# Kernel tuning notes

Measured on AMD Instinct MI355X. Metric: run time of the kernel, lower is better.

The kernel has to match this reference:

```python
import jax, jax.numpy as jnp
import numpy as np

N = 100000
E = 1600000
F_IN = 128
H = 256
C = 40
BN_EPS = 1e-5


def setup_inputs() -> dict:
    key = jax.random.key(0)
    ks = jax.random.split(key, 16)
    x = jax.random.normal(ks[0], (N, F_IN), dtype=jnp.float32)
    edge_index = jax.random.randint(ks[1], (2, E), 0, N, dtype=jnp.int64)
    # pre layer
    pre_w = jax.random.normal(ks[2], (H, F_IN), dtype=jnp.float32) * (1.0 / np.sqrt(F_IN))
    pre_b = jnp.zeros((H,), jnp.float32)
    # batchnorm params stacked [5, 4, H]: gamma, beta, running_mean, running_var
    gamma = jnp.ones((5, H), jnp.float32)
    beta = jnp.zeros((5, H), jnp.float32)
    rmean = jax.random.normal(ks[3], (5, H), dtype=jnp.float32) * 0.1
    rvar = jax.random.uniform(ks[4], (5, H), dtype=jnp.float32) * 0.5 + 0.5
    bn_params = jnp.stack([gamma, beta, rmean, rvar], axis=1)  # [5,4,H]
    # 3 SAGEConv layers: lin_l (neighbor, with bias), lin_r (root, no bias)
    s = 1.0 / np.sqrt(H)
    lin_l_w = jax.random.normal(ks[5], (3, H, H), dtype=jnp.float32) * s
    lin_l_b = jnp.zeros((3, H), jnp.float32)
    lin_r_w = jax.random.normal(ks[6], (3, H, H), dtype=jnp.float32) * s
    # post layers
    post1_w = jax.random.normal(ks[7], (H, H), dtype=jnp.float32) * s
    post1_b = jnp.zeros((H,), jnp.float32)
    post2_w = jax.random.normal(ks[8], (C, H), dtype=jnp.float32) * s
    post2_b = jnp.zeros((C,), jnp.float32)
    return {
        "x": x, "edge_index": edge_index,
        "pre_w": pre_w, "pre_b": pre_b, "bn_params": bn_params,
        "lin_l_w": lin_l_w, "lin_l_b": lin_l_b, "lin_r_w": lin_r_w,
        "post1_w": post1_w, "post1_b": post1_b,
        "post2_w": post2_w, "post2_b": post2_b,
    }


def _bn(x, p):
    # eval-mode BatchNorm1d with running stats; p: [4, H]
    g, b, m, v = p[0], p[1], p[2], p[3]
    return (x - m) * (g * jax.lax.rsqrt(v + BN_EPS)) + b


def _sage_conv(x, src, dst, wl, bl, wr):
    # PyG SAGEConv (aggr='mean'): lin_l(mean_{j in N(i)} x_j) + lin_r(x_i)
    msg = x[src]                                             # [E, H] gather
    agg = jax.ops.segment_sum(msg, dst, num_segments=N)       # [N, H] scatter
    cnt = jax.ops.segment_sum(jnp.ones((src.shape[0],), x.dtype), dst, num_segments=N)
    mean = agg / jnp.maximum(cnt, 1.0)[:, None]
    return mean @ wl.T + bl + x @ wr.T


def reference(x, edge_index, pre_w, pre_b, bn_params, lin_l_w, lin_l_b, lin_r_w,
              post1_w, post1_b, post2_w, post2_b):
    src, dst = edge_index[0], edge_index[1]
    h = x @ pre_w.T + pre_b
    h = jax.nn.relu(_bn(h, bn_params[0]))  # dropout is identity in eval mode
    for i in range(3):
        h = _sage_conv(h, src, dst, lin_l_w[i], lin_l_b[i], lin_r_w[i])
        h = jax.nn.relu(_bn(h, bn_params[i + 1]))
    h = h @ post1_w.T + post1_b
    h = jax.nn.relu(_bn(h, bn_params[4]))
    logits = h @ post2_w.T + post2_b
    return jax.nn.log_softmax(logits, axis=1)
```

## Files before the change

### kernel.cpp

```cpp
#include <hip/hip_runtime.h>
#include <cstdint>
#include <cstddef>

#define N_NODES 100000
#define N_EDGES 1600000
#define F_INDIM 128
#define HDIM 256
#define C_OUT 40
#define BN_EPS 1e-5f

typedef unsigned short bf16_t;
typedef __attribute__((ext_vector_type(8))) short bf16x8;
typedef __attribute__((ext_vector_type(4))) float f32x4;

__device__ __forceinline__ float bf2f(unsigned int u) {
  return __uint_as_float(u << 16);
}
__device__ __forceinline__ bf16_t f2bf(float f) {
  unsigned int x = __float_as_uint(f);
  return (bf16_t)((x + 0x7fffu + ((x >> 16) & 1u)) >> 16);
}

__global__ void k_cvt(const float* __restrict__ s, bf16_t* __restrict__ d, int n) {
  int i = (blockIdx.x * blockDim.x + threadIdx.x) * 4;
  if (i >= n) return;
  float4 v = *reinterpret_cast<const float4*>(&s[i]);
  uint2 o;
  o.x = (unsigned)f2bf(v.x) | ((unsigned)f2bf(v.y) << 16);
  o.y = (unsigned)f2bf(v.z) | ((unsigned)f2bf(v.w) << 16);
  *reinterpret_cast<uint2*>(&d[i]) = o;
}

__global__ void k_rank(const int* __restrict__ dst, int* __restrict__ cursor,
                       int* __restrict__ rank, int E) {
  for (int e = blockIdx.x * blockDim.x + threadIdx.x; e < E; e += gridDim.x * blockDim.x)
    rank[e] = atomicAdd(&cursor[dst[e]], 1);
}

__global__ __launch_bounds__(1024)
void k_scan_local(const int* __restrict__ cnt, int* __restrict__ row_ptr,
                  int* __restrict__ blk_sum, int n) {
  __shared__ int buf[1024];
  int tid = threadIdx.x;
  int i = blockIdx.x * 1024 + tid;
  int v = (i < n) ? cnt[i] : 0;
  buf[tid] = v;
  __syncthreads();
  for (int off = 1; off < 1024; off <<= 1) {
    int t = (tid >= off) ? buf[tid - off] : 0;
    __syncthreads();
    buf[tid] += t;
    __syncthreads();
  }
  if (i < n) row_ptr[i] = buf[tid] - v;
  if (tid == 1023) blk_sum[blockIdx.x] = buf[1023];
}

__global__ __launch_bounds__(128)
void k_scan_blk(const int* __restrict__ blk_sum, int* __restrict__ blk_off, int nb) {
  __shared__ int buf[128];
  int tid = threadIdx.x;
  int v = (tid < nb) ? blk_sum[tid] : 0;
  buf[tid] = v;
  __syncthreads();
  for (int off = 1; off < 128; off <<= 1) {
    int t = (tid >= off) ? buf[tid - off] : 0;
    __syncthreads();
    buf[tid] += t;
    __syncthreads();
  }
  if (tid < nb) blk_off[tid] = buf[tid] - v;
}

__global__ void k_scan_add(int* __restrict__ row_ptr, const int* __restrict__ blk_off, int n) {
  int i = blockIdx.x * blockDim.x + threadIdx.x;
  if (i < n) row_ptr[i] += blk_off[i >> 10];
  if (i == 0) row_ptr[n] = N_EDGES;
}

__global__ void k_place(const int* __restrict__ src, const int* __restrict__ dst,
                        const int* __restrict__ rank, const int* __restrict__ row_ptr,
                        int* __restrict__ csr, int E) {
  for (int e = blockIdx.x * blockDim.x + threadIdx.x; e < E; e += gridDim.x * blockDim.x)
    csr[row_ptr[dst[e]] + rank[e]] = src[e];
}

__global__ void k_inv(const int* __restrict__ cnt, float* __restrict__ inv, int n) {
  int i = blockIdx.x * blockDim.x + threadIdx.x;
  if (i < n) inv[i] = 1.0f / (float)(cnt[i] > 0 ? cnt[i] : 1);
}

__device__ __forceinline__ void add8(float* acc, uint4 r) {
  acc[0] += bf2f(r.x & 0xffffu); acc[1] += bf2f(r.x >> 16);
  acc[2] += bf2f(r.y & 0xffffu); acc[3] += bf2f(r.y >> 16);
  acc[4] += bf2f(r.z & 0xffffu); acc[5] += bf2f(r.z >> 16);
  acc[6] += bf2f(r.w & 0xffffu); acc[7] += bf2f(r.w >> 16);
}

__global__ __launch_bounds__(256)
void k_aggregate(const bf16_t* __restrict__ h, const int* __restrict__ row_ptr,
                 const int* __restrict__ csr, const float* __restrict__ inv_deg,
                 bf16_t* __restrict__ mean) {
  int w = threadIdx.x >> 6, lane = threadIdx.x & 63;
  int node = blockIdx.x * 4 + w;
  if (node >= N_NODES) return;
  int beg = row_ptr[node], end = row_ptr[node + 1];
  int half = lane >> 5;
  int l32 = lane & 31;
  float acc[8] = {};
  int deg = end - beg;
  int p = beg;
  int p8 = beg + (deg & ~7);
  for (; p < p8; p += 8) {
    int s0 = csr[p + half];
    int s1 = csr[p + 2 + half];
    int s2 = csr[p + 4 + half];
    int s3 = csr[p + 6 + half];
    uint4 r0 = *reinterpret_cast<const uint4*>(&h[(size_t)s0 * HDIM + l32 * 8]);
    uint4 r1 = *reinterpret_cast<const uint4*>(&h[(size_t)s1 * HDIM + l32 * 8]);
    uint4 r2 = *reinterpret_cast<const uint4*>(&h[(size_t)s2 * HDIM + l32 * 8]);
    uint4 r3 = *reinterpret_cast<const uint4*>(&h[(size_t)s3 * HDIM + l32 * 8]);
    add8(acc, r0);
    add8(acc, r1);
    add8(acc, r2);
    add8(acc, r3);
  }
  if (end - p >= 4) {
    int s0 = csr[p + half];
    int s1 = csr[p + 2 + half];
    uint4 r0 = *reinterpret_cast<const uint4*>(&h[(size_t)s0 * HDIM + l32 * 8]);
    uint4 r1 = *reinterpret_cast<const uint4*>(&h[(size_t)s1 * HDIM + l32 * 8]);
    add8(acc, r0);
    add8(acc, r1);
    p += 4;
  }
  for (; p < end; p += 2) {
    int e = p + half;
    if (e < end) {
      int s = csr[e];
      uint4 r = *reinterpret_cast<const uint4*>(&h[(size_t)s * HDIM + l32 * 8]);
      add8(acc, r);
    }
  }
#pragma unroll
  for (int k = 0; k < 8; ++k) acc[k] += __shfl_xor(acc[k], 32);
  if (half == 0) {
    float iv = inv_deg[node];
    uint4 o;
    o.x = (unsigned)f2bf(acc[0] * iv) | ((unsigned)f2bf(acc[1] * iv) << 16);
    o.y = (unsigned)f2bf(acc[2] * iv) | ((unsigned)f2bf(acc[3] * iv) << 16);
    o.z = (unsigned)f2bf(acc[4] * iv) | ((unsigned)f2bf(acc[5] * iv) << 16);
    o.w = (unsigned)f2bf(acc[6] * iv) | ((unsigned)f2bf(acc[7] * iv) << 16);
    *reinterpret_cast<uint4*>(&mean[(size_t)node * HDIM + l32 * 8]) = o;
  }
}

__device__ __forceinline__ void store1(float* p, float v) { *p = v; }
__device__ __forceinline__ void store1(bf16_t* p, float v) { *p = f2bf(v); }

template <typename TOUT>
__global__ __launch_bounds__(256)
void gemm_mfma(const bf16_t* __restrict__ A0, const bf16_t* __restrict__ W0,
               const bf16_t* __restrict__ A1, const bf16_t* __restrict__ W1,
               const float* __restrict__ bias, const float* __restrict__ bn,
               TOUT* __restrict__ C, int M, int K, int OUT, int dual) {
  __shared__ bf16_t lds[2][2][128 * 32];
  const int tid = threadIdx.x;
  const int lane = tid & 63, wid = tid >> 6;
  const int wm = wid >> 1, wn = wid & 1;
  const int row0 = blockIdx.x * 128, col0 = blockIdx.y * 128;
  const int l15 = lane & 15, l4 = lane >> 4;

  const int nk = K / 32;
  const int nsteps = dual ? nk * 2 : nk;

  f32x4 acc[4][4] = {};

  const int srow_base = wid * 32 + (lane >> 2);
  const int skk = ((lane & 3) ^ ((lane >> 3) & 3)) * 8;

  auto stage = [&](int s, int b) {
    const bf16_t* A = (s < nk) ? A0 : A1;
    const bf16_t* W = (s < nk) ? W0 : W1;
    int kk0 = ((s < nk) ? s : s - nk) * 32 + skk;
#pragma unroll
    for (int c = 0; c < 2; ++c) {
      int chunk = wid * 2 + c;
      int row = srow_base + c * 16;
      int ar = row0 + row; if (ar >= M) ar = M - 1;
      int br = col0 + row; if (br >= OUT) br = OUT - 1;
      __builtin_amdgcn_global_load_lds(
          (const __attribute__((address_space(1))) unsigned int*)&A[(size_t)ar * K + kk0],
          (__attribute__((address_space(3))) unsigned int*)&lds[b][0][chunk * 512],
          16, 0, 0);
      __builtin_amdgcn_global_load_lds(
          (const __attribute__((address_space(1))) unsigned int*)&W[(size_t)br * K + kk0],
          (__attribute__((address_space(3))) unsigned int*)&lds[b][1][chunk * 512],
          16, 0, 0);
    }
  };

  const int rslot = (l4 ^ ((l15 >> 1) & 3)) * 8;

  stage(0, 0);
  __syncthreads();
  int cur = 0;
  for (int s = 0; s < nsteps; ++s) {
    if (s + 1 < nsteps) stage(s + 1, cur ^ 1);
    const bf16_t* pa = &lds[cur][0][l15 * 32 + rslot];
    const bf16_t* pb = &lds[cur][1][l15 * 32 + rslot];
    bf16x8 a[4], b[4];
#pragma unroll
    for (int i = 0; i < 4; ++i)
      a[i] = *reinterpret_cast<const bf16x8*>(&pa[(wm * 64 + i * 16) * 32]);
#pragma unroll
    for (int j = 0; j < 4; ++j)
      b[j] = *reinterpret_cast<const bf16x8*>(&pb[(wn * 64 + j * 16) * 32]);
#pragma unroll
    for (int i = 0; i < 4; ++i)
#pragma unroll
      for (int j = 0; j < 4; ++j)
        acc[i][j] = __builtin_amdgcn_mfma_f32_16x16x32_bf16(a[i], b[j], acc[i][j], 0, 0, 0);
    if (s + 1 < nsteps) {
      __syncthreads();
      cur ^= 1;
    }
  }

#pragma unroll
  for (int j = 0; j < 4; ++j) {
    int col = col0 + wn * 64 + j * 16 + l15;
    if (col >= OUT) continue;
    float bs = bias ? bias[col] : 0.f;
    float scale = 1.f, shift = bs;
    bool has_bn = (bn != nullptr);
    if (has_bn) {
      float g = bn[col], bb = bn[256 + col], mm = bn[512 + col], vv = bn[768 + col];
      float is = g * rsqrtf(vv + BN_EPS);
      scale = is; shift = (bs - mm) * is + bb;
    }
#pragma unroll
    for (int i = 0; i < 4; ++i) {
#pragma unroll
      for (int r = 0; r < 4; ++r) {
        int row = row0 + wm * 64 + i * 16 + l4 * 4 + r;
        if (row >= M) continue;
        float v = acc[i][j][r];
        v = has_bn ? fmaxf(v * scale + shift, 0.f) : (v + bs);
        store1(&C[(size_t)row * OUT + col], v);
      }
    }
  }
}

__global__ __launch_bounds__(256)
void k_logsoftmax(const float* __restrict__ logits, float* __restrict__ out, int M) {
  int row = blockIdx.x * 4 + (threadIdx.x >> 6);
  if (row >= M) return;
  int lane = threadIdx.x & 63;
  float v = (lane < C_OUT) ? logits[(size_t)row * C_OUT + lane] : -1e30f;
  float m = v;
#pragma unroll
  for (int o = 32; o; o >>= 1) m = fmaxf(m, __shfl_xor(m, o));
  float e = (lane < C_OUT) ? expf(v - m) : 0.f;
  float s = e;
#pragma unroll
  for (int o = 32; o; o >>= 1) s += __shfl_xor(s, o);
  if (lane < C_OUT) out[(size_t)row * C_OUT + lane] = v - m - logf(s);
}

extern "C" void kernel_launch(void* const* d_in, const int* in_sizes, int n_in,
                              void* d_out, int out_size, void* d_ws, size_t ws_size,
                              hipStream_t stream) {
  const float* x       = (const float*)d_in[0];
  const int*   ei      = (const int*)d_in[1];
  const float* pre_w   = (const float*)d_in[2];
  const float* pre_b   = (const float*)d_in[3];
  const float* bn      = (const float*)d_in[4];
  const float* lin_l_w = (const float*)d_in[5];
  const float* lin_l_b = (const float*)d_in[6];
  const float* lin_r_w = (const float*)d_in[7];
  const float* post1_w = (const float*)d_in[8];
  const float* post1_b = (const float*)d_in[9];
  const float* post2_w = (const float*)d_in[10];
  const float* post2_b = (const float*)d_in[11];
  float* out = (float*)d_out;

  const int* src = ei;
  const int* dstv = ei + N_EDGES;

  char* base = (char*)d_ws;
  size_t off = 0;
  auto alloc = [&](size_t bytes) -> void* {
    void* p = base + off;
    off = (off + bytes + 255) & ~(size_t)255;
    return p;
  };
  bf16_t* hA = (bf16_t*)alloc((size_t)N_NODES * HDIM * 2);
  bf16_t* hB = (bf16_t*)alloc((size_t)N_NODES * HDIM * 2);
  bf16_t* hC = (bf16_t*)alloc((size_t)N_NODES * HDIM * 2);
  int* row_ptr = (int*)alloc((size_t)(N_NODES + 1) * 4);
  int* cursor  = (int*)alloc((size_t)N_NODES * 4);
  int* csr     = (int*)alloc((size_t)N_EDGES * 4);
  int* rank    = (int*)alloc((size_t)N_EDGES * 4);
  float* inv   = (float*)alloc((size_t)N_NODES * 4);
  int* blk_sum = (int*)alloc(128 * 4);
  int* blk_off = (int*)alloc(128 * 4);
  bf16_t* w_pre = (bf16_t*)alloc((size_t)HDIM * F_INDIM * 2);
  bf16_t* w_ll  = (bf16_t*)alloc((size_t)3 * HDIM * HDIM * 2);
  bf16_t* w_lr  = (bf16_t*)alloc((size_t)3 * HDIM * HDIM * 2);
  bf16_t* w_p1  = (bf16_t*)alloc((size_t)HDIM * HDIM * 2);
  bf16_t* w_p2  = (bf16_t*)alloc((size_t)C_OUT * HDIM * 2);
  (void)n_in; (void)in_sizes; (void)out_size;
  if (off > ws_size) return;

  bf16_t* x_bf = hB;

  {
    int n;
    n = N_NODES * F_INDIM;
    k_cvt<<<(n / 4 + 255) / 256, 256, 0, stream>>>(x, x_bf, n);
    n = HDIM * F_INDIM;
    k_cvt<<<(n / 4 + 255) / 256, 256, 0, stream>>>(pre_w, w_pre, n);
    n = 3 * HDIM * HDIM;
    k_cvt<<<(n / 4 + 255) / 256, 256, 0, stream>>>(lin_l_w, w_ll, n);
    k_cvt<<<(n / 4 + 255) / 256, 256, 0, stream>>>(lin_r_w, w_lr, n);
    n = HDIM * HDIM;
    k_cvt<<<(n / 4 + 255) / 256, 256, 0, stream>>>(post1_w, w_p1, n);
    n = C_OUT * HDIM;
    k_cvt<<<(n / 4 + 255) / 256, 256, 0, stream>>>(post2_w, w_p2, n);
  }

  hipMemsetAsync(cursor, 0, (size_t)N_NODES * 4, stream);
  k_rank<<<2048, 256, 0, stream>>>(dstv, cursor, rank, N_EDGES);
  int nb = (N_NODES + 1023) / 1024;
  k_scan_local<<<nb, 1024, 0, stream>>>(cursor, row_ptr, blk_sum, N_NODES);
  k_scan_blk<<<1, 128, 0, stream>>>(blk_sum, blk_off, nb);
  k_scan_add<<<(N_NODES + 255) / 256, 256, 0, stream>>>(row_ptr, blk_off, N_NODES);
  k_place<<<2048, 256, 0, stream>>>(src, dstv, rank, row_ptr, csr, N_EDGES);
  k_inv<<<(N_NODES + 255) / 256, 256, 0, stream>>>(cursor, inv, N_NODES);

  dim3 gH((N_NODES + 127) / 128, 2);
  gemm_mfma<bf16_t><<<gH, 256, 0, stream>>>(
      x_bf, w_pre, nullptr, nullptr, pre_b, bn, hA, N_NODES, F_INDIM, HDIM, 0);

  bf16_t* hcur = hA;
  bf16_t* hnext = hC;
  for (int i = 0; i < 3; ++i) {
    k_aggregate<<<N_NODES / 4, 256, 0, stream>>>(hcur, row_ptr, csr, inv, hB);
    gemm_mfma<bf16_t><<<gH, 256, 0, stream>>>(
        hB, w_ll + (size_t)i * HDIM * HDIM,
        hcur, w_lr + (size_t)i * HDIM * HDIM,
        lin_l_b + (size_t)i * HDIM,
        bn + (size_t)(i + 1) * 4 * HDIM,
        hnext, N_NODES, HDIM, HDIM, 1);
    bf16_t* t = hcur; hcur = hnext; hnext = t;
  }
  gemm_mfma<bf16_t><<<gH, 256, 0, stream>>>(
      hcur, w_p1, nullptr, nullptr, post1_b,
      bn + (size_t)4 * 4 * HDIM, hnext, N_NODES, HDIM, HDIM, 0);
  float* logits = (float*)hB;
  dim3 gC((N_NODES + 127) / 128, 1);
  gemm_mfma<float><<<gC, 256, 0, stream>>>(
      hnext, w_p2, nullptr, nullptr, post2_b,
      nullptr, logits, N_NODES, HDIM, C_OUT, 0);
  k_logsoftmax<<<(N_NODES + 3) / 4, 256, 0, stream>>>(logits, out, N_NODES);
}
```

Measured before the change: 783.0 us.

## Fuse neighbor mean aggregation into SAGE dual GEMM via LDS-resident tile

Replaces the separate aggregate kernel and dual-input GEMM with one kernel per SAGE layer. Each 512-thread block gathers the mean of 64 nodes into a swizzled LDS tile, then runs MFMA over the full 256 output columns. For the root term it reads A fragments of h straight from global memory. This removes the round trip of the mean buffer through HBM and one launch per layer. In exchange the gather phase is serialized before the GEMM in each block, the root-term A loads are uncached direct global reads, and LDS use per block rises, which may limit occupancy.

```diff
diff --git a/kernel.cpp b/kernel.cpp
--- a/kernel.cpp
+++ b/kernel.cpp
@@ -97,61 +97,144 @@
   acc[6] += bf2f(r.w & 0xffffu); acc[7] += bf2f(r.w >> 16);
 }
 
-__global__ __launch_bounds__(256)
-void k_aggregate(const bf16_t* __restrict__ h, const int* __restrict__ row_ptr,
-                 const int* __restrict__ csr, const float* __restrict__ inv_deg,
-                 bf16_t* __restrict__ mean) {
-  int w = threadIdx.x >> 6, lane = threadIdx.x & 63;
-  int node = blockIdx.x * 4 + w;
-  if (node >= N_NODES) return;
-  int beg = row_ptr[node], end = row_ptr[node + 1];
-  int half = lane >> 5;
-  int l32 = lane & 31;
-  float acc[8] = {};
-  int deg = end - beg;
-  int p = beg;
-  int p8 = beg + (deg & ~7);
-  for (; p < p8; p += 8) {
-    int s0 = csr[p + half];
-    int s1 = csr[p + 2 + half];
-    int s2 = csr[p + 4 + half];
-    int s3 = csr[p + 6 + half];
-    uint4 r0 = *reinterpret_cast<const uint4*>(&h[(size_t)s0 * HDIM + l32 * 8]);
-    uint4 r1 = *reinterpret_cast<const uint4*>(&h[(size_t)s1 * HDIM + l32 * 8]);
-    uint4 r2 = *reinterpret_cast<const uint4*>(&h[(size_t)s2 * HDIM + l32 * 8]);
-    uint4 r3 = *reinterpret_cast<const uint4*>(&h[(size_t)s3 * HDIM + l32 * 8]);
-    add8(acc, r0);
-    add8(acc, r1);
-    add8(acc, r2);
-    add8(acc, r3);
-  }
-  if (end - p >= 4) {
-    int s0 = csr[p + half];
-    int s1 = csr[p + 2 + half];
-    uint4 r0 = *reinterpret_cast<const uint4*>(&h[(size_t)s0 * HDIM + l32 * 8]);
-    uint4 r1 = *reinterpret_cast<const uint4*>(&h[(size_t)s1 * HDIM + l32 * 8]);
-    add8(acc, r0);
-    add8(acc, r1);
-    p += 4;
-  }
-  for (; p < end; p += 2) {
-    int e = p + half;
-    if (e < end) {
-      int s = csr[e];
-      uint4 r = *reinterpret_cast<const uint4*>(&h[(size_t)s * HDIM + l32 * 8]);
-      add8(acc, r);
-    }
-  }
-#pragma unroll
-  for (int k = 0; k < 8; ++k) acc[k] += __shfl_xor(acc[k], 32);
-  if (half == 0) {
-    float iv = inv_deg[node];
-    uint4 o;
-    o.x = (unsigned)f2bf(acc[0] * iv) | ((unsigned)f2bf(acc[1] * iv) << 16);
-    o.y = (unsigned)f2bf(acc[2] * iv) | ((unsigned)f2bf(acc[3] * iv) << 16);
-    o.z = (unsigned)f2bf(acc[4] * iv) | ((unsigned)f2bf(acc[5] * iv) << 16);
-    o.w = (unsigned)f2bf(acc[6] * iv) | ((unsigned)f2bf(acc[7] * iv) << 16);
-    *reinterpret_cast<uint4*>(&mean[(size_t)node * HDIM + l32 * 8]) = o;
+__global__ __launch_bounds__(512, 4)
+void fused_sage(const bf16_t* __restrict__ h, const int* __restrict__ row_ptr,
+                const int* __restrict__ csr, const float* __restrict__ inv_deg,
+                const bf16_t* __restrict__ wl, const bf16_t* __restrict__ wr,
+                const float* __restrict__ bias, const float* __restrict__ bn,
+                bf16_t* __restrict__ hnext, int M) {
+  __shared__ bf16_t meanL[64 * 256];
+  __shared__ bf16_t ldsB[2][256 * 32];
+  const int tid = threadIdx.x;
+  const int lane = tid & 63, wid = tid >> 6;
+  const int wm = wid >> 2, wn = wid & 3;
+  const int row0 = blockIdx.x * 64;
+  const int l15 = lane & 15, l4 = lane >> 4;
+
+  const int skk = ((lane & 3) ^ ((lane >> 3) & 3)) * 8;
+
+  auto stageB = [&](int s, int b) {
+    const bf16_t* W = (s < 8) ? wl : wr;
+    int kk0 = ((s < 8) ? s : s - 8) * 32 + skk;
+#pragma unroll
+    for (int c = 0; c < 2; ++c) {
+      int chunk = wid * 2 + c;
+      int br = chunk * 16 + (lane >> 2);
+      __builtin_amdgcn_global_load_lds(
+          (const __attribute__((address_space(1))) unsigned int*)&W[(size_t)br * HDIM + kk0],
+          (__attribute__((address_space(3))) unsigned int*)&ldsB[b][chunk * 512],
+          16, 0, 0);
+    }
+  };
+
+  stageB(0, 0);
+
+  {
+    int half = lane >> 5, l32 = lane & 31;
+    for (int t = 0; t < 8; ++t) {
+      int node = row0 + wid * 8 + t;
+      if (node >= M) break;
+      int beg = row_ptr[node], end = row_ptr[node + 1];
+      float acc[8] = {};
+      int p = beg;
+      int p8 = beg + ((end - beg) & ~7);
+      for (; p < p8; p += 8) {
+        int s0 = csr[p + half];
+        int s1 = csr[p + 2 + half];
+        int s2 = csr[p + 4 + half];
+        int s3 = csr[p + 6 + half];
+        uint4 r0 = *reinterpret_cast<const uint4*>(&h[(size_t)s0 * HDIM + l32 * 8]);
+        uint4 r1 = *reinterpret_cast<const uint4*>(&h[(size_t)s1 * HDIM + l32 * 8]);
+        uint4 r2 = *reinterpret_cast<const uint4*>(&h[(size_t)s2 * HDIM + l32 * 8]);
+        uint4 r3 = *reinterpret_cast<const uint4*>(&h[(size_t)s3 * HDIM + l32 * 8]);
+        add8(acc, r0); add8(acc, r1); add8(acc, r2); add8(acc, r3);
+      }
+      if (end - p >= 4) {
+        int s0 = csr[p + half];
+        int s1 = csr[p + 2 + half];
+        uint4 r0 = *reinterpret_cast<const uint4*>(&h[(size_t)s0 * HDIM + l32 * 8]);
+        uint4 r1 = *reinterpret_cast<const uint4*>(&h[(size_t)s1 * HDIM + l32 * 8]);
+        add8(acc, r0); add8(acc, r1);
+        p += 4;
+      }
+      for (; p < end; p += 2) {
+        int e = p + half;
+        if (e < end) {
+          int s = csr[e];
+          uint4 r = *reinterpret_cast<const uint4*>(&h[(size_t)s * HDIM + l32 * 8]);
+          add8(acc, r);
+        }
+      }
+#pragma unroll
+      for (int k = 0; k < 8; ++k) acc[k] += __shfl_xor(acc[k], 32);
+      if (half == 0) {
+        float iv = inv_deg[node];
+        uint4 o;
+        o.x = (unsigned)f2bf(acc[0] * iv) | ((unsigned)f2bf(acc[1] * iv) << 16);
+        o.y = (unsigned)f2bf(acc[2] * iv) | ((unsigned)f2bf(acc[3] * iv) << 16);
+        o.z = (unsigned)f2bf(acc[4] * iv) | ((unsigned)f2bf(acc[5] * iv) << 16);
+        o.w = (unsigned)f2bf(acc[6] * iv) | ((unsigned)f2bf(acc[7] * iv) << 16);
+        int r = wid * 8 + t;
+        int ps = l32 ^ (r & 7);
+        *reinterpret_cast<uint4*>(&meanL[r * 256 + ps * 8]) = o;
+      }
+    }
+  }
+  __syncthreads();
+
+  f32x4 acc[2][4] = {};
+  const int rslot = (l4 ^ ((l15 >> 1) & 3)) * 8;
+  int cur = 0;
+  for (int s = 0; s < 16; ++s) {
+    if (s + 1 < 16) stageB(s + 1, cur ^ 1);
+    bf16x8 bfr[4];
+    const bf16_t* pb = &ldsB[cur][l15 * 32 + rslot];
+#pragma unroll
+    for (int j = 0; j < 4; ++j)
+      bfr[j] = *reinterpret_cast<const bf16x8*>(&pb[(wn * 64 + j * 16) * 32]);
+    bf16x8 afr[2];
+    if (s < 8) {
+#pragma unroll
+      for (int i = 0; i < 2; ++i) {
+        int r = wm * 32 + i * 16 + l15;
+        int ps = (s * 4 + l4) ^ (r & 7);
+        afr[i] = *reinterpret_cast<const bf16x8*>(&meanL[r * 256 + ps * 8]);
+      }
+    } else {
+      int kk = (s - 8) * 32 + l4 * 8;
+#pragma unroll
+      for (int i = 0; i < 2; ++i) {
+        int gr = row0 + wm * 32 + i * 16 + l15; if (gr >= M) gr = M - 1;
+        afr[i] = *reinterpret_cast<const bf16x8*>(&h[(size_t)gr * HDIM + kk]);
+      }
+    }
+#pragma unroll
+    for (int i = 0; i < 2; ++i)
+#pragma unroll
+      for (int j = 0; j < 4; ++j)
+        acc[i][j] = __builtin_amdgcn_mfma_f32_16x16x32_bf16(afr[i], bfr[j], acc[i][j], 0, 0, 0);
+    if (s + 1 < 16) {
+      __syncthreads();
+      cur ^= 1;
+    }
+  }
+
+#pragma unroll
+  for (int j = 0; j < 4; ++j) {
+    int col = wn * 64 + j * 16 + l15;
+    float g = bn[col], bb = bn[256 + col], mm = bn[512 + col], vv = bn[768 + col];
+    float is = g * rsqrtf(vv + BN_EPS);
+    float scale = is, shift = (bias[col] - mm) * is + bb;
+#pragma unroll
+    for (int i = 0; i < 2; ++i) {
+#pragma unroll
+      for (int r = 0; r < 4; ++r) {
+        int row = row0 + wm * 32 + i * 16 + l4 * 4 + r;
+        if (row >= M) continue;
+        float v = fmaxf(acc[i][j][r] * scale + shift, 0.f);
+        hnext[(size_t)row * HDIM + col] = f2bf(v);
+      }
+    }
   }
 }
 
@@ -161,9 +244,8 @@
 template <typename TOUT>
 __global__ __launch_bounds__(256)
 void gemm_mfma(const bf16_t* __restrict__ A0, const bf16_t* __restrict__ W0,
-               const bf16_t* __restrict__ A1, const bf16_t* __restrict__ W1,
                const float* __restrict__ bias, const float* __restrict__ bn,
-               TOUT* __restrict__ C, int M, int K, int OUT, int dual) {
+               TOUT* __restrict__ C, int M, int K, int OUT) {
   __shared__ bf16_t lds[2][2][128 * 32];
   const int tid = threadIdx.x;
   const int lane = tid & 63, wid = tid >> 6;
@@ -172,17 +254,13 @@
   const int l15 = lane & 15, l4 = lane >> 4;
 
   const int nk = K / 32;
-  const int nsteps = dual ? nk * 2 : nk;
-
   f32x4 acc[4][4] = {};
 
   const int srow_base = wid * 32 + (lane >> 2);
   const int skk = ((lane & 3) ^ ((lane >> 3) & 3)) * 8;
 
   auto stage = [&](int s, int b) {
-    const bf16_t* A = (s < nk) ? A0 : A1;
-    const bf16_t* W = (s < nk) ? W0 : W1;
-    int kk0 = ((s < nk) ? s : s - nk) * 32 + skk;
+    int kk0 = s * 32 + skk;
 #pragma unroll
     for (int c = 0; c < 2; ++c) {
       int chunk = wid * 2 + c;
@@ -190,11 +268,11 @@
       int ar = row0 + row; if (ar >= M) ar = M - 1;
       int br = col0 + row; if (br >= OUT) br = OUT - 1;
       __builtin_amdgcn_global_load_lds(
-          (const __attribute__((address_space(1))) unsigned int*)&A[(size_t)ar * K + kk0],
+          (const __attribute__((address_space(1))) unsigned int*)&A0[(size_t)ar * K + kk0],
           (__attribute__((address_space(3))) unsigned int*)&lds[b][0][chunk * 512],
           16, 0, 0);
       __builtin_amdgcn_global_load_lds(
-          (const __attribute__((address_space(1))) unsigned int*)&W[(size_t)br * K + kk0],
+          (const __attribute__((address_space(1))) unsigned int*)&W0[(size_t)br * K + kk0],
           (__attribute__((address_space(3))) unsigned int*)&lds[b][1][chunk * 512],
           16, 0, 0);
     }
@@ -205,8 +283,8 @@
   stage(0, 0);
   __syncthreads();
   int cur = 0;
-  for (int s = 0; s < nsteps; ++s) {
-    if (s + 1 < nsteps) stage(s + 1, cur ^ 1);
+  for (int s = 0; s < nk; ++s) {
+    if (s + 1 < nk) stage(s + 1, cur ^ 1);
     const bf16_t* pa = &lds[cur][0][l15 * 32 + rslot];
     const bf16_t* pb = &lds[cur][1][l15 * 32 + rslot];
     bf16x8 a[4], b[4];
@@ -221,7 +299,7 @@
 #pragma unroll
       for (int j = 0; j < 4; ++j)
         acc[i][j] = __builtin_amdgcn_mfma_f32_16x16x32_bf16(a[i], b[j], acc[i][j], 0, 0, 0);
-    if (s + 1 < nsteps) {
+    if (s + 1 < nk) {
       __syncthreads();
       cur ^= 1;
     }
@@ -342,27 +420,24 @@
 
   dim3 gH((N_NODES + 127) / 128, 2);
   gemm_mfma<bf16_t><<<gH, 256, 0, stream>>>(
-      x_bf, w_pre, nullptr, nullptr, pre_b, bn, hA, N_NODES, F_INDIM, HDIM, 0);
+      x_bf, w_pre, pre_b, bn, hA, N_NODES, F_INDIM, HDIM);
 
   bf16_t* hcur = hA;
   bf16_t* hnext = hC;
+  int gF = (N_NODES + 63) / 64;
   for (int i = 0; i < 3; ++i) {
-    k_aggregate<<<N_NODES / 4, 256, 0, stream>>>(hcur, row_ptr, csr, inv, hB);
-    gemm_mfma<bf16_t><<<gH, 256, 0, stream>>>(
-        hB, w_ll + (size_t)i * HDIM * HDIM,
-        hcur, w_lr + (size_t)i * HDIM * HDIM,
-        lin_l_b + (size_t)i * HDIM,
-        bn + (size_t)(i + 1) * 4 * HDIM,
-        hnext, N_NODES, HDIM, HDIM, 1);
+    fused_sage<<<gF, 512, 0, stream>>>(
+        hcur, row_ptr, csr, inv,
+        w_ll + (size_t)i * HDIM * HDIM, w_lr + (size_t)i * HDIM * HDIM,
+        lin_l_b + (size_t)i * HDIM, bn + (size_t)(i + 1) * 4 * HDIM,
+        hnext, N_NODES);
     bf16_t* t = hcur; hcur = hnext; hnext = t;
   }
   gemm_mfma<bf16_t><<<gH, 256, 0, stream>>>(
-      hcur, w_p1, nullptr, nullptr, post1_b,
-      bn + (size_t)4 * 4 * HDIM, hnext, N_NODES, HDIM, HDIM, 0);
+      hcur, w_p1, post1_b, bn + (size_t)4 * 4 * HDIM, hnext, N_NODES, HDIM, HDIM);
   float* logits = (float*)hB;
   dim3 gC((N_NODES + 127) / 128, 1);
   gemm_mfma<float><<<gC, 256, 0, stream>>>(
-      hnext, w_p2, nullptr, nullptr, post2_b,
-      nullptr, logits, N_NODES, HDIM, C_OUT, 0);
+      hnext, w_p2, post2_b, nullptr, logits, N_NODES, HDIM, C_OUT);
   k_logsoftmax<<<(N_NODES + 3) / 4, 256, 0, stream>>>(logits, out, N_NODES);
 }
```

Result: slower. 805.9 us (+2.9%).
